# Kernel tuning notes

Hardware: AMD Instinct MI355X
Metric: run time of the kernel (lower is better)

## Reference

```python
import jax, jax.numpy as jnp
import numpy as np

LAMBD = 0.5
EPS = 1e-10


def setup_inputs() -> dict:
    key = jax.random.key(0)
    k1, k2 = jax.random.split(key)
    outputs = jax.random.uniform(k1, (64, 1000000), dtype=jnp.float32)
    labels = jax.random.randint(k2, (64, 1000000), 0, 2).astype(jnp.float32)
    return {"outputs": outputs, "labels": labels}


def reference(outputs, labels):
    # MSE loss (mean over all elements)
    mse = jnp.mean((outputs - labels) ** 2)

    # Vectorized confusion-matrix counts (replaces per-element Python loop).
    # pred = (outputs > 0.5); TP = sum(label==1 & pred==1); FN = sum(label==1 & pred==0)
    pred = (outputs > 0.5).astype(jnp.float32)
    TP = jnp.sum(labels * pred)
    FN = jnp.sum(labels * (1.0 - pred))

    # coeff = 1 if TP==0 and FN==0; 0 if TP==0 and FN!=0; else TP/(TP+FN)
    coeff = jnp.where(
        (TP == 0) & (FN == 0),
        jnp.float32(1.0),
        jnp.where(TP == 0, jnp.float32(0.0), TP / (TP + FN)),
    )
    cost_sensitive = -jnp.log(coeff + EPS)
    # In the original, this term is computed in numpy (no gradient flow)
    cost_sensitive = jax.lax.stop_gradient(cost_sensitive)

    return mse + LAMBD * cost_sensitive
```

## Files before the change

### kernel.cpp

```cpp
#include <hip/hip_runtime.h>
#include <math.h>

#define BLOCK 256
#define NBLOCKS 2048
#define UNROLL 4
#define EPS 1e-10f
#define LAMBD 0.5f

#define ACC(o, l)                                                         \
    do {                                                                  \
        float d0 = o.x - l.x, d1 = o.y - l.y;                             \
        float d2 = o.z - l.z, d3 = o.w - l.w;                             \
        sse += d0 * d0 + d1 * d1 + d2 * d2 + d3 * d3;                     \
        sl  += l.x + l.y + l.z + l.w;                                     \
        tp  += (o.x > 0.5f ? l.x : 0.f) + (o.y > 0.5f ? l.y : 0.f)        \
             + (o.z > 0.5f ? l.z : 0.f) + (o.w > 0.5f ? l.w : 0.f);       \
    } while (0)

__global__ __launch_bounds__(BLOCK, 4) void detloss_reduce(
    const float4* __restrict__ o4, const float4* __restrict__ l4,
    float* __restrict__ part, int n4, long long n,
    const float* __restrict__ outp, const float* __restrict__ lab) {

    float sse = 0.f, tp = 0.f, sl = 0.f;

    const int stride = gridDim.x * BLOCK;
    const int chunk  = stride * UNROLL;
    const int n_main = (n4 / chunk) * chunk;

    int i = blockIdx.x * BLOCK + threadIdx.x;

    for (; i < n_main; i += chunk) {
        float4 o0 = o4[i             ], l0 = l4[i             ];
        float4 o1 = o4[i +     stride], l1 = l4[i +     stride];
        float4 o2 = o4[i + 2 * stride], l2 = l4[i + 2 * stride];
        float4 o3 = o4[i + 3 * stride], l3 = l4[i + 3 * stride];
        __builtin_amdgcn_sched_barrier(0);
        ACC(o0, l0); ACC(o1, l1); ACC(o2, l2); ACC(o3, l3);
    }

    for (; i < n4; i += stride) {
        float4 o = o4[i], l = l4[i];
        ACC(o, l);
    }

    if (blockIdx.x == 0 && threadIdx.x == 0) {
        for (long long j = (long long)n4 << 2; j < n; ++j) {
            float o = outp[j], l = lab[j];
            float d = o - l;
            sse += d * d;
            sl  += l;
            tp  += (o > 0.5f ? l : 0.f);
        }
    }

    for (int off = 32; off > 0; off >>= 1) {
        sse += __shfl_down(sse, off);
        tp  += __shfl_down(tp,  off);
        sl  += __shfl_down(sl,  off);
    }

    __shared__ float s_sse[BLOCK / 64], s_tp[BLOCK / 64], s_sl[BLOCK / 64];
    const int lane = threadIdx.x & 63;
    const int wave = threadIdx.x >> 6;
    if (lane == 0) { s_sse[wave] = sse; s_tp[wave] = tp; s_sl[wave] = sl; }
    __syncthreads();

    if (threadIdx.x == 0) {
        float bsse = 0.f, btp = 0.f, bsl = 0.f;
        for (int w = 0; w < BLOCK / 64; ++w) {
            bsse += s_sse[w]; btp += s_tp[w]; bsl += s_sl[w];
        }
        const int nb = gridDim.x;
        part[blockIdx.x]          = bsse;
        part[nb + blockIdx.x]     = btp;
        part[2 * nb + blockIdx.x] = bsl;
    }
}

__global__ __launch_bounds__(256) void detloss_final(
    const float* __restrict__ part, int nblk,
    float* __restrict__ out, float inv_n) {

    float sse = 0.f, tp = 0.f, sl = 0.f;
    for (int i = threadIdx.x; i < nblk; i += 256) {
        sse += part[i];
        tp  += part[nblk + i];
        sl  += part[2 * nblk + i];
    }
    for (int off = 32; off > 0; off >>= 1) {
        sse += __shfl_down(sse, off);
        tp  += __shfl_down(tp,  off);
        sl  += __shfl_down(sl,  off);
    }
    __shared__ float s[3][4];
    const int lane = threadIdx.x & 63;
    const int wave = threadIdx.x >> 6;
    if (lane == 0) { s[0][wave] = sse; s[1][wave] = tp; s[2][wave] = sl; }
    __syncthreads();

    if (threadIdx.x == 0) {
        sse = s[0][0] + s[0][1] + s[0][2] + s[0][3];
        tp  = s[1][0] + s[1][1] + s[1][2] + s[1][3];
        sl  = s[2][0] + s[2][1] + s[2][2] + s[2][3];
        float fn = sl - tp;
        float coeff;
        if (tp == 0.f && fn == 0.f)      coeff = 1.f;
        else if (tp == 0.f)              coeff = 0.f;
        else                             coeff = tp / (tp + fn);
        float cost = -logf(coeff + EPS);
        out[0] = sse * inv_n + LAMBD * cost;
    }
}

extern "C" void kernel_launch(void* const* d_in, const int* in_sizes, int n_in,
                              void* d_out, int out_size, void* d_ws, size_t ws_size,
                              hipStream_t stream) {
    const float* outp = (const float*)d_in[0];
    const float* lab  = (const float*)d_in[1];
    float* out  = (float*)d_out;
    float* part = (float*)d_ws;

    long long n = (long long)in_sizes[0];
    int n4 = (int)(n >> 2);

    int blocks = (n4 + BLOCK - 1) / BLOCK;
    if (blocks > NBLOCKS) blocks = NBLOCKS;
    if (blocks < 1) blocks = 1;

    detloss_reduce<<<blocks, BLOCK, 0, stream>>>(
        (const float4*)outp, (const float4*)lab, part, n4, n, outp, lab);
    detloss_final<<<1, 256, 0, stream>>>(part, blocks, out, 1.0f / (float)n);
}
```

Measured before the change: 99.93 us.

## Fuse final reduction via last-block atomic counter and software-pipeline loads

Merges the two-kernel reduction into one kernel: each block writes its partials, increments an atomic counter, and the last block to finish performs the final reduction and loss computation. The main loop now handles 8 floats per thread per iteration and prefetches the next iteration's loads while accumulating the current ones, replacing the 4-way unrolled batch. This removes the second kernel launch but adds a hipMemsetAsync to reset the counter and leaves fewer loads in flight per thread than the previous unroll.

```diff
diff --git a/kernel.cpp b/kernel.cpp
--- a/kernel.cpp
+++ b/kernel.cpp
@@ -3,7 +3,6 @@
 
 #define BLOCK 256
 #define NBLOCKS 2048
-#define UNROLL 4
 #define EPS 1e-10f
 #define LAMBD 0.5f
 
@@ -17,35 +16,39 @@
              + (o.z > 0.5f ? l.z : 0.f) + (o.w > 0.5f ? l.w : 0.f);       \
     } while (0)
 
-__global__ __launch_bounds__(BLOCK, 4) void detloss_reduce(
+__global__ __launch_bounds__(BLOCK, 4) void detloss_fused(
     const float4* __restrict__ o4, const float4* __restrict__ l4,
-    float* __restrict__ part, int n4, long long n,
-    const float* __restrict__ outp, const float* __restrict__ lab) {
+    const float* __restrict__ outp, const float* __restrict__ lab,
+    float* __restrict__ part, unsigned int* __restrict__ counter,
+    float* __restrict__ out, int n8, long long n, float inv_n) {
 
     float sse = 0.f, tp = 0.f, sl = 0.f;
 
     const int stride = gridDim.x * BLOCK;
-    const int chunk  = stride * UNROLL;
-    const int n_main = (n4 / chunk) * chunk;
-
     int i = blockIdx.x * BLOCK + threadIdx.x;
 
-    for (; i < n_main; i += chunk) {
-        float4 o0 = o4[i             ], l0 = l4[i             ];
-        float4 o1 = o4[i +     stride], l1 = l4[i +     stride];
-        float4 o2 = o4[i + 2 * stride], l2 = l4[i + 2 * stride];
-        float4 o3 = o4[i + 3 * stride], l3 = l4[i + 3 * stride];
-        __builtin_amdgcn_sched_barrier(0);
-        ACC(o0, l0); ACC(o1, l1); ACC(o2, l2); ACC(o3, l3);
+    float4 co0, co1, cl0, cl1;
+    bool have = (i < n8);
+    if (have) {
+        co0 = o4[2 * i]; co1 = o4[2 * i + 1];
+        cl0 = l4[2 * i]; cl1 = l4[2 * i + 1];
     }
-
-    for (; i < n4; i += stride) {
-        float4 o = o4[i], l = l4[i];
-        ACC(o, l);
+    while (have) {
+        const int ni = i + stride;
+        const bool nhave = (ni < n8);
+        float4 no0 = co0, no1 = co1, nl0 = cl0, nl1 = cl1;
+        if (nhave) {
+            no0 = o4[2 * ni]; no1 = o4[2 * ni + 1];
+            nl0 = l4[2 * ni]; nl1 = l4[2 * ni + 1];
+        }
+        ACC(co0, cl0);
+        ACC(co1, cl1);
+        co0 = no0; co1 = no1; cl0 = nl0; cl1 = nl1;
+        i = ni; have = nhave;
     }
 
     if (blockIdx.x == 0 && threadIdx.x == 0) {
-        for (long long j = (long long)n4 << 2; j < n; ++j) {
+        for (long long j = (long long)n8 * 8; j < n; ++j) {
             float o = outp[j], l = lab[j];
             float d = o - l;
             sse += d * d;
@@ -61,55 +64,54 @@
     }
 
     __shared__ float s_sse[BLOCK / 64], s_tp[BLOCK / 64], s_sl[BLOCK / 64];
+    __shared__ bool s_last;
     const int lane = threadIdx.x & 63;
     const int wave = threadIdx.x >> 6;
     if (lane == 0) { s_sse[wave] = sse; s_tp[wave] = tp; s_sl[wave] = sl; }
     __syncthreads();
 
+    const int nb = gridDim.x;
     if (threadIdx.x == 0) {
         float bsse = 0.f, btp = 0.f, bsl = 0.f;
         for (int w = 0; w < BLOCK / 64; ++w) {
             bsse += s_sse[w]; btp += s_tp[w]; bsl += s_sl[w];
         }
-        const int nb = gridDim.x;
         part[blockIdx.x]          = bsse;
         part[nb + blockIdx.x]     = btp;
         part[2 * nb + blockIdx.x] = bsl;
+        __threadfence();
+        unsigned old = atomicAdd(counter, 1u);
+        s_last = (old == (unsigned)nb - 1u);
     }
-}
-
-__global__ __launch_bounds__(256) void detloss_final(
-    const float* __restrict__ part, int nblk,
-    float* __restrict__ out, float inv_n) {
-
-    float sse = 0.f, tp = 0.f, sl = 0.f;
-    for (int i = threadIdx.x; i < nblk; i += 256) {
-        sse += part[i];
-        tp  += part[nblk + i];
-        sl  += part[2 * nblk + i];
-    }
-    for (int off = 32; off > 0; off >>= 1) {
-        sse += __shfl_down(sse, off);
-        tp  += __shfl_down(tp,  off);
-        sl  += __shfl_down(sl,  off);
-    }
-    __shared__ float s[3][4];
-    const int lane = threadIdx.x & 63;
-    const int wave = threadIdx.x >> 6;
-    if (lane == 0) { s[0][wave] = sse; s[1][wave] = tp; s[2][wave] = sl; }
     __syncthreads();
 
-    if (threadIdx.x == 0) {
-        sse = s[0][0] + s[0][1] + s[0][2] + s[0][3];
-        tp  = s[1][0] + s[1][1] + s[1][2] + s[1][3];
-        sl  = s[2][0] + s[2][1] + s[2][2] + s[2][3];
-        float fn = sl - tp;
-        float coeff;
-        if (tp == 0.f && fn == 0.f)      coeff = 1.f;
-        else if (tp == 0.f)              coeff = 0.f;
-        else                             coeff = tp / (tp + fn);
-        float cost = -logf(coeff + EPS);
-        out[0] = sse * inv_n + LAMBD * cost;
+    if (s_last) {
+        __threadfence();
+        float fs = 0.f, ft = 0.f, fl = 0.f;
+        for (int k = threadIdx.x; k < nb; k += BLOCK) {
+            fs += part[k];
+            ft += part[nb + k];
+            fl += part[2 * nb + k];
+        }
+        for (int off = 32; off > 0; off >>= 1) {
+            fs += __shfl_down(fs, off);
+            ft += __shfl_down(ft, off);
+            fl += __shfl_down(fl, off);
+        }
+        __syncthreads();
+        if (lane == 0) { s_sse[wave] = fs; s_tp[wave] = ft; s_sl[wave] = fl; }
+        __syncthreads();
+        if (threadIdx.x == 0) {
+            float S = s_sse[0] + s_sse[1] + s_sse[2] + s_sse[3];
+            float T = s_tp[0]  + s_tp[1]  + s_tp[2]  + s_tp[3];
+            float L = s_sl[0]  + s_sl[1]  + s_sl[2]  + s_sl[3];
+            float fn = L - T;
+            float coeff;
+            if (T == 0.f && fn == 0.f)      coeff = 1.f;
+            else if (T == 0.f)              coeff = 0.f;
+            else                            coeff = T / (T + fn);
+            out[0] = S * inv_n + LAMBD * (-logf(coeff + EPS));
+        }
     }
 }
 
@@ -118,17 +120,21 @@
                               hipStream_t stream) {
     const float* outp = (const float*)d_in[0];
     const float* lab  = (const float*)d_in[1];
-    float* out  = (float*)d_out;
-    float* part = (float*)d_ws;
+    float* out = (float*)d_out;
+
+    unsigned int* counter = (unsigned int*)d_ws;
+    float* part = ((float*)d_ws) + 8;
 
     long long n = (long long)in_sizes[0];
-    int n4 = (int)(n >> 2);
+    int n8 = (int)(n >> 3);
 
-    int blocks = (n4 + BLOCK - 1) / BLOCK;
+    int blocks = (n8 + BLOCK - 1) / BLOCK;
     if (blocks > NBLOCKS) blocks = NBLOCKS;
     if (blocks < 1) blocks = 1;
 
-    detloss_reduce<<<blocks, BLOCK, 0, stream>>>(
-        (const float4*)outp, (const float4*)lab, part, n4, n, outp, lab);
-    detloss_final<<<1, 256, 0, stream>>>(part, blocks, out, 1.0f / (float)n);
+    hipMemsetAsync(counter, 0, sizeof(unsigned int), stream);
+
+    detloss_fused<<<blocks, BLOCK, 0, stream>>>(
+        (const float4*)outp, (const float4*)lab, outp, lab,
+        part, counter, out, n8, n, 1.0f / (float)n);
 }
```

Result: slower. 194.5 us (+94.6%).
